# Performance work log

Hardware: AMD Instinct MI355X
Metric: run time of the kernel (lower is better)

Reference implementation:

```python
import jax, jax.numpy as jnp
import numpy as np

N_NODES = 100000
N_EDGES = 1600000
IN_DIM, HID_DIM, OUT_DIM = 128, 128, 64


def setup_inputs() -> dict:
    key = jax.random.key(0)
    ks = jax.random.split(key, 5)
    x = jax.random.normal(ks[0], (N_NODES, IN_DIM), dtype=jnp.float32)
    edge_index = jax.random.randint(ks[1], (2, N_EDGES), 0, N_NODES, dtype=jnp.int64)
    W1 = jax.random.normal(ks[2], (IN_DIM, HID_DIM), dtype=jnp.float32) * (1.0 / np.sqrt(IN_DIM))
    b1 = jnp.zeros((HID_DIM,), dtype=jnp.float32)
    W2 = jax.random.normal(ks[3], (HID_DIM, OUT_DIM), dtype=jnp.float32) * (1.0 / np.sqrt(HID_DIM))
    b2 = jnp.zeros((OUT_DIM,), dtype=jnp.float32)
    return {"x": x, "edge_index": edge_index, "W1": W1, "b1": b1, "W2": W2, "b2": b2}


def _gcn_conv(h, row, col, norm, b, n_nodes):
    # h: [N, F] already linearly transformed; message = norm_e * h[src]; scatter-add to dst
    msg = h[row] * norm[:, None]                      # [E+N, F]
    out = jax.ops.segment_sum(msg, col, num_segments=n_nodes)
    return out + b


def reference(x, edge_index, W1, b1, W2, b2):
    n = x.shape[0]
    loops = jnp.arange(n, dtype=edge_index.dtype)
    row = jnp.concatenate([edge_index[0], loops])     # sources (incl. self loops)
    col = jnp.concatenate([edge_index[1], loops])     # targets
    # symmetric normalization: deg over targets with unit edge weights
    deg = jax.ops.segment_sum(jnp.ones_like(col, dtype=x.dtype), col, num_segments=n)
    dinv = jnp.where(deg > 0, jax.lax.rsqrt(jnp.maximum(deg, 1.0)), 0.0)
    norm = dinv[row] * dinv[col]                      # [E+N]
    h = jax.nn.relu(_gcn_conv(x @ W1, row, col, norm, b1, n))
    out = _gcn_conv(h @ W2, row, col, norm, b2, n)
    return out.mean(axis=0)                           # [OUT_DIM]
```

## Files before the change

kernel.cpp:

```cpp
#include <hip/hip_runtime.h>

#define N_NODES 100000
#define N_EDGES 1600000
#define IN_DIM 128
#define HID_DIM 128
#define OUT_DIM 64
#define BKT_SHIFT 8
#define BKT_SIZE 256
#define NBKT ((N_NODES + BKT_SIZE - 1) / BKT_SIZE)
#define B1 256
#define HIST_N (NBKT * B1)
#define HIST_N2 (2 * HIST_N)
#define GEMM_BLKS ((N_NODES + 127) / 128)

typedef float v2f __attribute__((ext_vector_type(2)));
typedef float v4f __attribute__((ext_vector_type(4)));
typedef short v8s __attribute__((ext_vector_type(8)));

__device__ __forceinline__ unsigned int f2bf(float f) {
  unsigned int u = __float_as_uint(f);
  return (u + 0x7FFFu + ((u >> 16) & 1u)) >> 16;
}

__device__ __forceinline__ void load4(const void* ei, int is64, int half, int base,
                                      int* v) {
  if (is64) {
    const long long* e = (const long long*)ei + (size_t)half * N_EDGES + base;
    longlong2 a = *(const longlong2*)e;
    longlong2 b = *(const longlong2*)(e + 2);
    v[0] = (int)a.x; v[1] = (int)a.y; v[2] = (int)b.x; v[3] = (int)b.y;
  } else {
    const int* e = (const int*)ei + (size_t)half * N_EDGES + base;
    int4 a = *(const int4*)e;
    v[0] = a.x; v[1] = a.y; v[2] = a.z; v[3] = a.w;
  }
}

__device__ __forceinline__ int detect64_block(const unsigned int* ei, int* sh) {
  if (threadIdx.x == 0) *sh = 0;
  __syncthreads();
  if (ei[1 + 2 * threadIdx.x] != 0u) *sh = 1;
  __syncthreads();
  return (*sh == 0) ? 1 : 0;
}

__global__ __launch_bounds__(256) void front_kernel(const float* __restrict__ x,
                                                    const float* __restrict__ W,
                                                    const void* ei,
                                                    unsigned int* __restrict__ G,
                                                    int* hist, float* S) {
  __shared__ __align__(16) char smem[2 * 128 * 136 * 2];
  if (blockIdx.x >= GEMM_BLKS) {
    int* hd = (int*)smem;
    int* hs = hd + NBKT;
    int* sh = hs + NBKT;
    const int hb = blockIdx.x - GEMM_BLKS;
    if (hb == 0 && threadIdx.x < HID_DIM) S[threadIdx.x] = 0.f;
    const int is64 = detect64_block((const unsigned int*)ei, sh);
    for (int k = threadIdx.x; k < NBKT; k += 256) { hd[k] = 0; hs[k] = 0; }
    __syncthreads();
    for (int g = hb * 256 + threadIdx.x; g < N_EDGES / 4; g += B1 * 256) {
      int r[4], c[4];
      load4(ei, is64, 0, g * 4, r);
      load4(ei, is64, 1, g * 4, c);
#pragma unroll
      for (int k = 0; k < 4; k++) {
        atomicAdd(&hd[c[k] >> BKT_SHIFT], 1);
        atomicAdd(&hs[r[k] >> BKT_SHIFT], 1);
      }
    }
    __syncthreads();
    for (int k = threadIdx.x; k < NBKT; k += 256) {
      hist[k * B1 + hb] = hd[k];
      hist[HIST_N + k * B1 + hb] = hs[k];
    }
    return;
  }
  typedef unsigned short us_row[136];
  us_row* lx = (us_row*)smem;
  us_row* lwt = (us_row*)(smem + 128 * 136 * 2);
  const int t = threadIdx.x;
  const int row0 = blockIdx.x * 128;

  {
    const float4* W4 = (const float4*)W;
    for (int it = 0; it < 16; ++it) {
      int idx = t + 256 * it;
      int k = idx >> 5, c4 = (idx & 31) * 4;
      float4 w = W4[idx];
      lwt[c4 + 0][k] = (unsigned short)f2bf(w.x);
      lwt[c4 + 1][k] = (unsigned short)f2bf(w.y);
      lwt[c4 + 2][k] = (unsigned short)f2bf(w.z);
      lwt[c4 + 3][k] = (unsigned short)f2bf(w.w);
    }
  }
  {
    const float4* x4 = (const float4*)(x + (size_t)row0 * IN_DIM);
    for (int it = 0; it < 16; ++it) {
      int idx = t + 256 * it;
      int r = idx >> 5, kq = (idx & 31) * 4;
      float4 v = make_float4(0.f, 0.f, 0.f, 0.f);
      if (row0 + r < N_NODES) v = x4[idx];
      unsigned int p0 = (f2bf(v.y) << 16) | f2bf(v.x);
      unsigned int p1 = (f2bf(v.w) << 16) | f2bf(v.z);
      *(uint2*)&lx[r][kq] = make_uint2(p0, p1);
    }
  }
  __syncthreads();

  const int lane = t & 63;
  const int wv = t >> 6;
  const int m0 = wv * 32;
  const int lrow = lane & 15;
  const int lk = (lane >> 4) * 8;

  v4f acc[2][8];
#pragma unroll
  for (int si = 0; si < 2; si++)
#pragma unroll
    for (int n = 0; n < 8; n++) acc[si][n] = (v4f){0.f, 0.f, 0.f, 0.f};

#pragma unroll
  for (int kk = 0; kk < 128; kk += 32) {
    v8s a0 = *(const v8s*)&lx[m0 + lrow][kk + lk];
    v8s a1 = *(const v8s*)&lx[m0 + 16 + lrow][kk + lk];
#pragma unroll
    for (int n = 0; n < 8; n++) {
      v8s b = *(const v8s*)&lwt[n * 16 + lrow][kk + lk];
      acc[0][n] = __builtin_amdgcn_mfma_f32_16x16x32_bf16(a0, b, acc[0][n], 0, 0, 0);
      acc[1][n] = __builtin_amdgcn_mfma_f32_16x16x32_bf16(a1, b, acc[1][n], 0, 0, 0);
    }
  }

  unsigned char* G8 = (unsigned char*)G;
#pragma unroll
  for (int si = 0; si < 2; si++)
#pragma unroll
    for (int n = 0; n < 8; n++) {
      int colg = n * 16 + (lane & 15);
#pragma unroll
      for (int i = 0; i < 4; i++) {
        int r = row0 + m0 + si * 16 + (lane >> 4) * 4 + i;
        if (r < N_NODES) {
          float v = acc[si][n][i];
          int pk = __builtin_amdgcn_cvt_pk_fp8_f32(v, v, 0, false);
          G8[(size_t)r * HID_DIM + colg] = (unsigned char)(pk & 0xFF);
        }
      }
    }
}

__global__ void scan1_kernel(int* arr, int* bsum, int n) {
  __shared__ int tmp[256];
  int i = blockIdx.x * 256 + threadIdx.x;
  int v = (i < n) ? arr[i] : 0;
  tmp[threadIdx.x] = v;
  __syncthreads();
  for (int off = 1; off < 256; off <<= 1) {
    int t2 = (threadIdx.x >= off) ? tmp[threadIdx.x - off] : 0;
    __syncthreads();
    tmp[threadIdx.x] += t2;
    __syncthreads();
  }
  if (i < n) arr[i] = tmp[threadIdx.x] - v;
  if (threadIdx.x == 255) bsum[blockIdx.x] = tmp[255];
}

__global__ void scan2_kernel(int* bsum, int nb) {
  __shared__ int tmp[1024];
  int v = (threadIdx.x < nb) ? bsum[threadIdx.x] : 0;
  tmp[threadIdx.x] = v;
  __syncthreads();
  for (int off = 1; off < 1024; off <<= 1) {
    int t2 = (threadIdx.x >= off) ? tmp[threadIdx.x - off] : 0;
    __syncthreads();
    tmp[threadIdx.x] += t2;
    __syncthreads();
  }
  if (threadIdx.x < nb) bsum[threadIdx.x] = tmp[threadIdx.x] - v;
}

__global__ __launch_bounds__(256) void scatter_kernel(const void* ei, const int* hist,
                                                      const int* bsum,
                                                      unsigned int* pairs) {
  __shared__ int cd[NBKT], cs[NBKT], sh[1];
  const int is64 = detect64_block((const unsigned int*)ei, sh);
  for (int k = threadIdx.x; k < NBKT; k += 256) {
    cd[k] = hist[k * B1 + blockIdx.x] + bsum[k];
    cs[k] = hist[HIST_N + k * B1 + blockIdx.x] + bsum[NBKT + k];
  }
  __syncthreads();
  for (int g = blockIdx.x * 256 + threadIdx.x; g < N_EDGES / 4; g += B1 * 256) {
    int r[4], c[4];
    load4(ei, is64, 0, g * 4, r);
    load4(ei, is64, 1, g * 4, c);
#pragma unroll
    for (int k = 0; k < 4; k++) {
      int pd = atomicAdd(&cd[c[k] >> BKT_SHIFT], 1);
      pairs[pd] = ((unsigned int)(c[k] & (BKT_SIZE - 1)) << 17) | (unsigned int)r[k];
      int ps = atomicAdd(&cs[r[k] >> BKT_SHIFT], 1);
      pairs[ps] = ((unsigned int)(r[k] & (BKT_SIZE - 1)) << 17) | (unsigned int)c[k];
    }
  }
}

__global__ __launch_bounds__(256) void csr_kernel(const int* hist, const int* bsum,
                                                  const unsigned int* pairs,
                                                  int* rowptr, int* csr, float* dinv) {
  __shared__ int cnt[BKT_SIZE], sc[BKT_SIZE], cur[BKT_SIZE];
  const int k = blockIdx.x;
  const int base = hist[k * B1] + bsum[k];
  const int end = (k == NBKT - 1) ? N_EDGES : hist[(k + 1) * B1] + bsum[k + 1];
  const int nseg = end - base;
  const int l = threadIdx.x;
  cnt[l] = 0;
  __syncthreads();
  for (int i = l; i < nseg; i += 256) atomicAdd(&cnt[pairs[base + i] >> 17], 1);
  __syncthreads();
  sc[l] = cnt[l];
  __syncthreads();
  for (int off = 1; off < BKT_SIZE; off <<= 1) {
    int v = (l >= off) ? sc[l - off] : 0;
    __syncthreads();
    sc[l] += v;
    __syncthreads();
  }
  {
    int excl = sc[l] - cnt[l];
    cur[l] = base + excl;
    int v = k * BKT_SIZE + l;
    if (v < N_NODES) {
      rowptr[v] = base + excl;
      dinv[v] = rsqrtf((float)(cnt[l] + 1));
    }
  }
  if (k == NBKT - 1 && l == 0) rowptr[N_NODES] = N_EDGES;
  __syncthreads();
  for (int i = l; i < nseg; i += 256) {
    unsigned int pk = pairs[base + i];
    int pos = atomicAdd(&cur[pk >> 17], 1);
    csr[pos] = (int)(pk & 0x1FFFFu);
  }
}

__global__ __launch_bounds__(256) void outsum_kernel(const int* hist, const int* bsum,
                                                     const unsigned int* pairs,
                                                     const float* __restrict__ dinv,
                                                     float* wacc,
                                                     unsigned int* __restrict__ G) {
  __shared__ float fb[BKT_SIZE];
  const int k = blockIdx.x;
  const int base = hist[HIST_N + k * B1] + bsum[NBKT + k];
  const int end =
      (k == NBKT - 1) ? 2 * N_EDGES : hist[HIST_N + (k + 1) * B1] + bsum[NBKT + k + 1];
  fb[threadIdx.x] = 0.f;
  __syncthreads();
  for (int i = base + threadIdx.x; i < end; i += 256) {
    unsigned int pk = pairs[i];
    atomicAdd(&fb[pk >> 17], dinv[pk & 0x1FFFFu]);
  }
  {
    const int j0 = k * BKT_SIZE * 32;
#pragma unroll
    for (int it = 0; it < 32; ++it) {
      int j = j0 + it * 256 + threadIdx.x;
      int node = j >> 5;
      if (node < N_NODES) {
        float d = dinv[node];
        unsigned int g = G[j];
        v2f lo = __builtin_amdgcn_cvt_pk_f32_fp8((int)g, false) * d;
        v2f hi = __builtin_amdgcn_cvt_pk_f32_fp8((int)g, true) * d;
        int pk2 = __builtin_amdgcn_cvt_pk_fp8_f32(lo.x, lo.y, 0, false);
        pk2 = __builtin_amdgcn_cvt_pk_fp8_f32(hi.x, hi.y, pk2, true);
        G[j] = (unsigned int)pk2;
      }
    }
  }
  __syncthreads();
  int v = k * BKT_SIZE + threadIdx.x;
  if (v < N_NODES) wacc[v] = fb[threadIdx.x];
}

__global__ __launch_bounds__(256) void aggregate_kernel(
    const unsigned int* __restrict__ G, const int* __restrict__ rowptr,
    const int* __restrict__ csr, const float* __restrict__ dinv,
    const float* __restrict__ wacc, const float* __restrict__ b1,
    float* __restrict__ S) {
  const int lane = threadIdx.x & 63;
  const int sub = lane & 31;
  const int half = lane >> 5;
  const int wid = blockIdx.x * (blockDim.x >> 6) + (threadIdx.x >> 6);
  const int nwaves = gridDim.x * (blockDim.x >> 6);
  const float4 b = ((const float4*)b1)[sub];
  v2f s01 = {0.f, 0.f}, s23 = {0.f, 0.f};

  for (int c = wid; c < N_NODES; c += nwaves) {
    const int start = rowptr[c];
    const int cnum = rowptr[c + 1] - start;
    v2f a01 = {0.f, 0.f}, a23 = {0.f, 0.f};
    if (half == 0) {
      unsigned int g = G[c * 32 + sub];
      a01 = __builtin_amdgcn_cvt_pk_f32_fp8((int)g, false);
      a23 = __builtin_amdgcn_cvt_pk_f32_fp8((int)g, true);
    }
    for (int j0 = 0; j0 < cnum; j0 += 64) {
      int src = 0;
      if (j0 + lane < cnum)
        src = __builtin_nontemporal_load(&csr[start + j0 + lane]);
      const int m = min(64, cnum - j0);
      int i = 0;
      for (; i + 8 <= m; i += 8) {
        int s0 = __shfl(src, i + half);
        int s1 = __shfl(src, i + 2 + half);
        int s2 = __shfl(src, i + 4 + half);
        int s3 = __shfl(src, i + 6 + half);
        unsigned int g0 = G[s0 * 32 + sub];
        unsigned int g1 = G[s1 * 32 + sub];
        unsigned int g2 = G[s2 * 32 + sub];
        unsigned int g3 = G[s3 * 32 + sub];
        a01 += __builtin_amdgcn_cvt_pk_f32_fp8((int)g0, false) +
               __builtin_amdgcn_cvt_pk_f32_fp8((int)g1, false);
        a23 += __builtin_amdgcn_cvt_pk_f32_fp8((int)g0, true) +
               __builtin_amdgcn_cvt_pk_f32_fp8((int)g1, true);
        a01 += __builtin_amdgcn_cvt_pk_f32_fp8((int)g2, false) +
               __builtin_amdgcn_cvt_pk_f32_fp8((int)g3, false);
        a23 += __builtin_amdgcn_cvt_pk_f32_fp8((int)g2, true) +
               __builtin_amdgcn_cvt_pk_f32_fp8((int)g3, true);
      }
      for (; i + 2 <= m; i += 2) {
        int s = __shfl(src, i + half);
        unsigned int g = G[s * 32 + sub];
        a01 += __builtin_amdgcn_cvt_pk_f32_fp8((int)g, false);
        a23 += __builtin_amdgcn_cvt_pk_f32_fp8((int)g, true);
      }
      if (i < m) {
        int s = __shfl(src, i);
        if (half == 0) {
          unsigned int g = G[s * 32 + sub];
          a01 += __builtin_amdgcn_cvt_pk_f32_fp8((int)g, false);
          a23 += __builtin_amdgcn_cvt_pk_f32_fp8((int)g, true);
        }
      }
    }
    a01.x += __shfl(a01.x, sub + 32);
    a01.y += __shfl(a01.y, sub + 32);
    a23.x += __shfl(a23.x, sub + 32);
    a23.y += __shfl(a23.y, sub + 32);
    if (half == 0) {
      float d = dinv[c];
      float wc = d * (wacc[c] + d);
      s01.x += wc * fmaxf(fmaf(d, a01.x, b.x), 0.f);
      s01.y += wc * fmaxf(fmaf(d, a01.y, b.y), 0.f);
      s23.x += wc * fmaxf(fmaf(d, a23.x, b.z), 0.f);
      s23.y += wc * fmaxf(fmaf(d, a23.y, b.w), 0.f);
    }
  }

  __shared__ float ls[HID_DIM];
  if (threadIdx.x < HID_DIM) ls[threadIdx.x] = 0.f;
  __syncthreads();
  if (half == 0) {
    atomicAdd(&ls[4 * sub + 0], s01.x);
    atomicAdd(&ls[4 * sub + 1], s01.y);
    atomicAdd(&ls[4 * sub + 2], s23.x);
    atomicAdd(&ls[4 * sub + 3], s23.y);
  }
  __syncthreads();
  if (threadIdx.x < HID_DIM) atomicAdd(&S[threadIdx.x], ls[threadIdx.x]);
}

__global__ void finish_kernel(const float* __restrict__ S, const float* __restrict__ W2,
                              const float* __restrict__ b2, float* __restrict__ out) {
  int j = threadIdx.x;
  float acc = 0.f;
  for (int k = 0; k < HID_DIM; k++) acc += S[k] * W2[k * OUT_DIM + j];
  out[j] = acc * (1.0f / N_NODES) + b2[j];
}

extern "C" void kernel_launch(void* const* d_in, const int* in_sizes, int n_in,
                              void* d_out, int out_size, void* d_ws, size_t ws_size,
                              hipStream_t stream) {
  const float* x  = (const float*)d_in[0];
  const void*  ei = d_in[1];
  const float* W1 = (const float*)d_in[2];
  const float* b1 = (const float*)d_in[3];
  const float* W2 = (const float*)d_in[4];
  const float* b2 = (const float*)d_in[5];
  float* out = (float*)d_out;

  char* p = (char*)d_ws;
  size_t off = 0;
  auto alloc = [&](size_t bytes) -> void* {
    void* r = p + off;
    off = (off + bytes + 63) & ~(size_t)63;
    return r;
  };
  int*   hist   = (int*)alloc((size_t)HIST_N2 * 4);
  int*   bsum   = (int*)alloc(1024 * 4);
  unsigned int* pairs = (unsigned int*)alloc((size_t)2 * N_EDGES * 4);
  int*   rowptr = (int*)alloc(((size_t)N_NODES + 1) * 4);
  int*   csr    = (int*)alloc((size_t)N_EDGES * 4);
  float* dinv   = (float*)alloc((size_t)N_NODES * 4);
  float* wacc   = (float*)alloc((size_t)N_NODES * 4);
  float* S      = (float*)alloc(HID_DIM * 4);
  unsigned int* G = (unsigned int*)alloc((size_t)N_NODES * HID_DIM);
  (void)ws_size; (void)n_in; (void)in_sizes; (void)out_size;

  const int NBH = HIST_N2 / 256;

  front_kernel<<<GEMM_BLKS + B1, 256, 0, stream>>>(x, W1, ei, G, hist, S);
  scan1_kernel<<<NBH, 256, 0, stream>>>(hist, bsum, HIST_N2);
  scan2_kernel<<<1, 1024, 0, stream>>>(bsum, NBH);
  scatter_kernel<<<B1, 256, 0, stream>>>(ei, hist, bsum, pairs);
  csr_kernel<<<NBKT, 256, 0, stream>>>(hist, bsum, pairs, rowptr, csr, dinv);
  outsum_kernel<<<NBKT, 256, 0, stream>>>(hist, bsum, pairs, dinv, wacc, G);
  aggregate_kernel<<<2048, 256, 0, stream>>>(G, rowptr, csr, dinv, wacc, b1, S);
  finish_kernel<<<1, 64, 0, stream>>>(S, W2, b2, out);
}
```

Measured before the change: 290.7 us.

## Pack source dinv as bf16 into CSR entries instead of rescaling G

The outsum kernel no longer rescales the fp8 feature matrix G by dinv in place (a read-modify-write of G with an fp8 requantisation). It instead writes a bf16-rounded dinv of each source into the upper bits of its CSR entry. The aggregate kernel then reads each neighbour's weight straight from the packed index and multiplies during accumulation. It also loads 8 bytes per lane as uint2, so 16 lanes cover a row and four edges are gathered per wave step instead of two. This removes one pass over G and one fp8 rounding step, in exchange for more multiplies in the gather loop and bf16 precision on the weights.

```diff
diff --git a/kernel.cpp b/kernel.cpp
--- a/kernel.cpp
+++ b/kernel.cpp
@@ -20,6 +20,11 @@
 __device__ __forceinline__ unsigned int f2bf(float f) {
   unsigned int u = __float_as_uint(f);
   return (u + 0x7FFFu + ((u >> 16) & 1u)) >> 16;
+}
+
+template <bool HI>
+__device__ __forceinline__ v2f cvt8(unsigned int u) {
+  return __builtin_amdgcn_cvt_pk_f32_fp8((int)u, HI);
 }
 
 __device__ __forceinline__ void load4(const void* ei, int is64, int half, int base,
@@ -206,7 +211,8 @@
 
 __global__ __launch_bounds__(256) void csr_kernel(const int* hist, const int* bsum,
                                                   const unsigned int* pairs,
-                                                  int* rowptr, int* csr, float* dinv) {
+                                                  int* rowptr, unsigned int* csr,
+                                                  float* dinv) {
   __shared__ int cnt[BKT_SIZE], sc[BKT_SIZE], cur[BKT_SIZE];
   const int k = blockIdx.x;
   const int base = hist[k * B1] + bsum[k];
@@ -239,7 +245,7 @@
   for (int i = l; i < nseg; i += 256) {
     unsigned int pk = pairs[base + i];
     int pos = atomicAdd(&cur[pk >> 17], 1);
-    csr[pos] = (int)(pk & 0x1FFFFu);
+    csr[pos] = pk & 0x1FFFFu;
   }
 }
 
@@ -247,7 +253,7 @@
                                                      const unsigned int* pairs,
                                                      const float* __restrict__ dinv,
                                                      float* wacc,
-                                                     unsigned int* __restrict__ G) {
+                                                     unsigned int* __restrict__ csr) {
   __shared__ float fb[BKT_SIZE];
   const int k = blockIdx.x;
   const int base = hist[HIST_N + k * B1] + bsum[NBKT + k];
@@ -259,22 +265,10 @@
     unsigned int pk = pairs[i];
     atomicAdd(&fb[pk >> 17], dinv[pk & 0x1FFFFu]);
   }
-  {
-    const int j0 = k * BKT_SIZE * 32;
-#pragma unroll
-    for (int it = 0; it < 32; ++it) {
-      int j = j0 + it * 256 + threadIdx.x;
-      int node = j >> 5;
-      if (node < N_NODES) {
-        float d = dinv[node];
-        unsigned int g = G[j];
-        v2f lo = __builtin_amdgcn_cvt_pk_f32_fp8((int)g, false) * d;
-        v2f hi = __builtin_amdgcn_cvt_pk_f32_fp8((int)g, true) * d;
-        int pk2 = __builtin_amdgcn_cvt_pk_fp8_f32(lo.x, lo.y, 0, false);
-        pk2 = __builtin_amdgcn_cvt_pk_fp8_f32(hi.x, hi.y, pk2, true);
-        G[j] = (unsigned int)pk2;
-      }
-    }
+  for (int i = blockIdx.x * 256 + threadIdx.x; i < N_EDGES; i += NBKT * 256) {
+    unsigned int src = csr[i] & 0x1FFFFu;
+    unsigned int bits = f2bf(dinv[src]);
+    csr[i] = (bits << 17) | src;
   }
   __syncthreads();
   int v = k * BKT_SIZE + threadIdx.x;
@@ -282,88 +276,97 @@
 }
 
 __global__ __launch_bounds__(256) void aggregate_kernel(
-    const unsigned int* __restrict__ G, const int* __restrict__ rowptr,
-    const int* __restrict__ csr, const float* __restrict__ dinv,
+    const uint2* __restrict__ G2, const int* __restrict__ rowptr,
+    const unsigned int* __restrict__ csr, const float* __restrict__ dinv,
     const float* __restrict__ wacc, const float* __restrict__ b1,
     float* __restrict__ S) {
   const int lane = threadIdx.x & 63;
-  const int sub = lane & 31;
-  const int half = lane >> 5;
-  const int wid = blockIdx.x * (blockDim.x >> 6) + (threadIdx.x >> 6);
-  const int nwaves = gridDim.x * (blockDim.x >> 6);
-  const float4 b = ((const float4*)b1)[sub];
-  v2f s01 = {0.f, 0.f}, s23 = {0.f, 0.f};
+  const int q = lane & 15;
+  const int grp = lane >> 4;
+  const int wid = blockIdx.x * 4 + (threadIdx.x >> 6);
+  const int nwaves = gridDim.x * 4;
+  const float2* b2p = (const float2*)b1;
+  const float2 bb0 = b2p[q * 4 + 0], bb1 = b2p[q * 4 + 1];
+  const float2 bb2 = b2p[q * 4 + 2], bb3 = b2p[q * 4 + 3];
+  v2f s0 = {0.f, 0.f}, s1 = {0.f, 0.f}, s2 = {0.f, 0.f}, s3 = {0.f, 0.f};
 
   for (int c = wid; c < N_NODES; c += nwaves) {
     const int start = rowptr[c];
     const int cnum = rowptr[c + 1] - start;
-    v2f a01 = {0.f, 0.f}, a23 = {0.f, 0.f};
-    if (half == 0) {
-      unsigned int g = G[c * 32 + sub];
-      a01 = __builtin_amdgcn_cvt_pk_f32_fp8((int)g, false);
-      a23 = __builtin_amdgcn_cvt_pk_f32_fp8((int)g, true);
+    const float d = dinv[c];
+    v2f a0 = {0.f, 0.f}, a1 = {0.f, 0.f}, a2 = {0.f, 0.f}, a3 = {0.f, 0.f};
+    if (grp == 0) {
+      uint2 g = G2[c * 16 + q];
+      a0 = cvt8<false>(g.x) * d;
+      a1 = cvt8<true>(g.x) * d;
+      a2 = cvt8<false>(g.y) * d;
+      a3 = cvt8<true>(g.y) * d;
     }
     for (int j0 = 0; j0 < cnum; j0 += 64) {
-      int src = 0;
+      unsigned int pkl = 0;
       if (j0 + lane < cnum)
-        src = __builtin_nontemporal_load(&csr[start + j0 + lane]);
+        pkl = __builtin_nontemporal_load(&csr[start + j0 + lane]);
       const int m = min(64, cnum - j0);
       int i = 0;
-      for (; i + 8 <= m; i += 8) {
-        int s0 = __shfl(src, i + half);
-        int s1 = __shfl(src, i + 2 + half);
-        int s2 = __shfl(src, i + 4 + half);
-        int s3 = __shfl(src, i + 6 + half);
-        unsigned int g0 = G[s0 * 32 + sub];
-        unsigned int g1 = G[s1 * 32 + sub];
-        unsigned int g2 = G[s2 * 32 + sub];
-        unsigned int g3 = G[s3 * 32 + sub];
-        a01 += __builtin_amdgcn_cvt_pk_f32_fp8((int)g0, false) +
-               __builtin_amdgcn_cvt_pk_f32_fp8((int)g1, false);
-        a23 += __builtin_amdgcn_cvt_pk_f32_fp8((int)g0, true) +
-               __builtin_amdgcn_cvt_pk_f32_fp8((int)g1, true);
-        a01 += __builtin_amdgcn_cvt_pk_f32_fp8((int)g2, false) +
-               __builtin_amdgcn_cvt_pk_f32_fp8((int)g3, false);
-        a23 += __builtin_amdgcn_cvt_pk_f32_fp8((int)g2, true) +
-               __builtin_amdgcn_cvt_pk_f32_fp8((int)g3, true);
+      for (; i + 16 <= m; i += 16) {
+        unsigned int p0 = __shfl(pkl, i + grp);
+        unsigned int p1 = __shfl(pkl, i + 4 + grp);
+        unsigned int p2 = __shfl(pkl, i + 8 + grp);
+        unsigned int p3 = __shfl(pkl, i + 12 + grp);
+        uint2 g0 = G2[(p0 & 0x1FFFFu) * 16 + q];
+        uint2 g1 = G2[(p1 & 0x1FFFFu) * 16 + q];
+        uint2 g2 = G2[(p2 & 0x1FFFFu) * 16 + q];
+        uint2 g3 = G2[(p3 & 0x1FFFFu) * 16 + q];
+        float w0 = __uint_as_float((p0 >> 17) << 16);
+        float w1 = __uint_as_float((p1 >> 17) << 16);
+        float w2 = __uint_as_float((p2 >> 17) << 16);
+        float w3 = __uint_as_float((p3 >> 17) << 16);
+        a0 += cvt8<false>(g0.x) * w0; a1 += cvt8<true>(g0.x) * w0;
+        a2 += cvt8<false>(g0.y) * w0; a3 += cvt8<true>(g0.y) * w0;
+        a0 += cvt8<false>(g1.x) * w1; a1 += cvt8<true>(g1.x) * w1;
+        a2 += cvt8<false>(g1.y) * w1; a3 += cvt8<true>(g1.y) * w1;
+        a0 += cvt8<false>(g2.x) * w2; a1 += cvt8<true>(g2.x) * w2;
+        a2 += cvt8<false>(g2.y) * w2; a3 += cvt8<true>(g2.y) * w2;
+        a0 += cvt8<false>(g3.x) * w3; a1 += cvt8<true>(g3.x) * w3;
+        a2 += cvt8<false>(g3.y) * w3; a3 += cvt8<true>(g3.y) * w3;
       }
-      for (; i + 2 <= m; i += 2) {
-        int s = __shfl(src, i + half);
-        unsigned int g = G[s * 32 + sub];
-        a01 += __builtin_amdgcn_cvt_pk_f32_fp8((int)g, false);
-        a23 += __builtin_amdgcn_cvt_pk_f32_fp8((int)g, true);
+      for (; i < m; i += 4) {
+        int e = i + grp;
+        unsigned int pv = __shfl(pkl, min(e, m - 1));
+        float w = (e < m) ? __uint_as_float((pv >> 17) << 16) : 0.f;
+        uint2 g = G2[(pv & 0x1FFFFu) * 16 + q];
+        a0 += cvt8<false>(g.x) * w; a1 += cvt8<true>(g.x) * w;
+        a2 += cvt8<false>(g.y) * w; a3 += cvt8<true>(g.y) * w;
       }
-      if (i < m) {
-        int s = __shfl(src, i);
-        if (half == 0) {
-          unsigned int g = G[s * 32 + sub];
-          a01 += __builtin_amdgcn_cvt_pk_f32_fp8((int)g, false);
-          a23 += __builtin_amdgcn_cvt_pk_f32_fp8((int)g, true);
-        }
-      }
-    }
-    a01.x += __shfl(a01.x, sub + 32);
-    a01.y += __shfl(a01.y, sub + 32);
-    a23.x += __shfl(a23.x, sub + 32);
-    a23.y += __shfl(a23.y, sub + 32);
-    if (half == 0) {
-      float d = dinv[c];
+    }
+#pragma unroll
+    for (int off = 16; off < 64; off <<= 1) {
+      a0.x += __shfl_xor(a0.x, off); a0.y += __shfl_xor(a0.y, off);
+      a1.x += __shfl_xor(a1.x, off); a1.y += __shfl_xor(a1.y, off);
+      a2.x += __shfl_xor(a2.x, off); a2.y += __shfl_xor(a2.y, off);
+      a3.x += __shfl_xor(a3.x, off); a3.y += __shfl_xor(a3.y, off);
+    }
+    if (grp == 0) {
       float wc = d * (wacc[c] + d);
-      s01.x += wc * fmaxf(fmaf(d, a01.x, b.x), 0.f);
-      s01.y += wc * fmaxf(fmaf(d, a01.y, b.y), 0.f);
-      s23.x += wc * fmaxf(fmaf(d, a23.x, b.z), 0.f);
-      s23.y += wc * fmaxf(fmaf(d, a23.y, b.w), 0.f);
+      s0.x += wc * fmaxf(fmaf(d, a0.x, bb0.x), 0.f);
+      s0.y += wc * fmaxf(fmaf(d, a0.y, bb0.y), 0.f);
+      s1.x += wc * fmaxf(fmaf(d, a1.x, bb1.x), 0.f);
+      s1.y += wc * fmaxf(fmaf(d, a1.y, bb1.y), 0.f);
+      s2.x += wc * fmaxf(fmaf(d, a2.x, bb2.x), 0.f);
+      s2.y += wc * fmaxf(fmaf(d, a2.y, bb2.y), 0.f);
+      s3.x += wc * fmaxf(fmaf(d, a3.x, bb3.x), 0.f);
+      s3.y += wc * fmaxf(fmaf(d, a3.y, bb3.y), 0.f);
     }
   }
 
   __shared__ float ls[HID_DIM];
   if (threadIdx.x < HID_DIM) ls[threadIdx.x] = 0.f;
   __syncthreads();
-  if (half == 0) {
-    atomicAdd(&ls[4 * sub + 0], s01.x);
-    atomicAdd(&ls[4 * sub + 1], s01.y);
-    atomicAdd(&ls[4 * sub + 2], s23.x);
-    atomicAdd(&ls[4 * sub + 3], s23.y);
+  if (grp == 0) {
+    atomicAdd(&ls[8 * q + 0], s0.x); atomicAdd(&ls[8 * q + 1], s0.y);
+    atomicAdd(&ls[8 * q + 2], s1.x); atomicAdd(&ls[8 * q + 3], s1.y);
+    atomicAdd(&ls[8 * q + 4], s2.x); atomicAdd(&ls[8 * q + 5], s2.y);
+    atomicAdd(&ls[8 * q + 6], s3.x); atomicAdd(&ls[8 * q + 7], s3.y);
   }
   __syncthreads();
   if (threadIdx.x < HID_DIM) atomicAdd(&S[threadIdx.x], ls[threadIdx.x]);
@@ -399,7 +402,7 @@
   int*   bsum   = (int*)alloc(1024 * 4);
   unsigned int* pairs = (unsigned int*)alloc((size_t)2 * N_EDGES * 4);
   int*   rowptr = (int*)alloc(((size_t)N_NODES + 1) * 4);
-  int*   csr    = (int*)alloc((size_t)N_EDGES * 4);
+  unsigned int* csr = (unsigned int*)alloc((size_t)N_EDGES * 4);
   float* dinv   = (float*)alloc((size_t)N_NODES * 4);
   float* wacc   = (float*)alloc((size_t)N_NODES * 4);
   float* S      = (float*)alloc(HID_DIM * 4);
@@ -413,7 +416,8 @@
   scan2_kernel<<<1, 1024, 0, stream>>>(bsum, NBH);
   scatter_kernel<<<B1, 256, 0, stream>>>(ei, hist, bsum, pairs);
   csr_kernel<<<NBKT, 256, 0, stream>>>(hist, bsum, pairs, rowptr, csr, dinv);
-  outsum_kernel<<<NBKT, 256, 0, stream>>>(hist, bsum, pairs, dinv, wacc, G);
-  aggregate_kernel<<<2048, 256, 0, stream>>>(G, rowptr, csr, dinv, wacc, b1, S);
+  outsum_kernel<<<NBKT, 256, 0, stream>>>(hist, bsum, pairs, dinv, wacc, csr);
+  aggregate_kernel<<<2048, 256, 0, stream>>>((const uint2*)G, rowptr, csr, dinv, wacc,
+                                             b1, S);
   finish_kernel<<<1, 64, 0, stream>>>(S, W2, b2, out);
 }
```

Measured after the change: 290.8 us. No clear change (+0.0%).

## Pack source dinv as bf16 weight into CSR entries instead of rescaling G

Applied to the files above, without the earlier changes.

Stops rescaling the fp8 feature matrix G by dinv in outsum_kernel. Instead it encodes each edge's source dinv as a truncated bf16 in the upper 15 bits of the CSR index word, and the aggregation multiplies each gathered row by that weight. This removes the read-modify-write pass over G and the extra fp8 requantisation, which should also improve accuracy. In exchange it adds a pass over the CSR array and per-edge multiplies in the gather loop. The weight loses precision because only 15 bits are kept (the bf16 sign bit is dropped).

```diff
diff --git a/kernel.cpp b/kernel.cpp
--- a/kernel.cpp
+++ b/kernel.cpp
@@ -20,6 +20,15 @@
 __device__ __forceinline__ unsigned int f2bf(float f) {
   unsigned int u = __float_as_uint(f);
   return (u + 0x7FFFu + ((u >> 16) & 1u)) >> 16;
+}
+
+template <bool HI>
+__device__ __forceinline__ v2f cvt8(unsigned int u) {
+  return __builtin_amdgcn_cvt_pk_f32_fp8((int)u, HI);
+}
+
+__device__ __forceinline__ float wdec(unsigned int p) {
+  return __uint_as_float((p >> 17) << 16);
 }
 
 __device__ __forceinline__ void load4(const void* ei, int is64, int half, int base,
@@ -206,7 +215,8 @@
 
 __global__ __launch_bounds__(256) void csr_kernel(const int* hist, const int* bsum,
                                                   const unsigned int* pairs,
-                                                  int* rowptr, int* csr, float* dinv) {
+                                                  int* rowptr, unsigned int* csr,
+                                                  float* dinv) {
   __shared__ int cnt[BKT_SIZE], sc[BKT_SIZE], cur[BKT_SIZE];
   const int k = blockIdx.x;
   const int base = hist[k * B1] + bsum[k];
@@ -239,7 +249,7 @@
   for (int i = l; i < nseg; i += 256) {
     unsigned int pk = pairs[base + i];
     int pos = atomicAdd(&cur[pk >> 17], 1);
-    csr[pos] = (int)(pk & 0x1FFFFu);
+    csr[pos] = pk & 0x1FFFFu;
   }
 }
 
@@ -247,7 +257,7 @@
                                                      const unsigned int* pairs,
                                                      const float* __restrict__ dinv,
                                                      float* wacc,
-                                                     unsigned int* __restrict__ G) {
+                                                     unsigned int* __restrict__ csr) {
   __shared__ float fb[BKT_SIZE];
   const int k = blockIdx.x;
   const int base = hist[HIST_N + k * B1] + bsum[NBKT + k];
@@ -259,22 +269,10 @@
     unsigned int pk = pairs[i];
     atomicAdd(&fb[pk >> 17], dinv[pk & 0x1FFFFu]);
   }
-  {
-    const int j0 = k * BKT_SIZE * 32;
-#pragma unroll
-    for (int it = 0; it < 32; ++it) {
-      int j = j0 + it * 256 + threadIdx.x;
-      int node = j >> 5;
-      if (node < N_NODES) {
-        float d = dinv[node];
-        unsigned int g = G[j];
-        v2f lo = __builtin_amdgcn_cvt_pk_f32_fp8((int)g, false) * d;
-        v2f hi = __builtin_amdgcn_cvt_pk_f32_fp8((int)g, true) * d;
-        int pk2 = __builtin_amdgcn_cvt_pk_fp8_f32(lo.x, lo.y, 0, false);
-        pk2 = __builtin_amdgcn_cvt_pk_fp8_f32(hi.x, hi.y, pk2, true);
-        G[j] = (unsigned int)pk2;
-      }
-    }
+  for (int i = blockIdx.x * 256 + threadIdx.x; i < N_EDGES; i += NBKT * 256) {
+    unsigned int src = __builtin_nontemporal_load(&csr[i]) & 0x1FFFFu;
+    unsigned int bits = f2bf(dinv[src]);
+    __builtin_nontemporal_store((bits << 17) | src, &csr[i]);
   }
   __syncthreads();
   int v = k * BKT_SIZE + threadIdx.x;
@@ -283,62 +281,62 @@
 
 __global__ __launch_bounds__(256) void aggregate_kernel(
     const unsigned int* __restrict__ G, const int* __restrict__ rowptr,
-    const int* __restrict__ csr, const float* __restrict__ dinv,
+    const unsigned int* __restrict__ csr, const float* __restrict__ dinv,
     const float* __restrict__ wacc, const float* __restrict__ b1,
     float* __restrict__ S) {
   const int lane = threadIdx.x & 63;
   const int sub = lane & 31;
   const int half = lane >> 5;
-  const int wid = blockIdx.x * (blockDim.x >> 6) + (threadIdx.x >> 6);
-  const int nwaves = gridDim.x * (blockDim.x >> 6);
+  const int wid = blockIdx.x * 4 + (threadIdx.x >> 6);
+  const int nwaves = gridDim.x * 4;
   const float4 b = ((const float4*)b1)[sub];
   v2f s01 = {0.f, 0.f}, s23 = {0.f, 0.f};
 
   for (int c = wid; c < N_NODES; c += nwaves) {
     const int start = rowptr[c];
     const int cnum = rowptr[c + 1] - start;
+    const float d = dinv[c];
     v2f a01 = {0.f, 0.f}, a23 = {0.f, 0.f};
     if (half == 0) {
       unsigned int g = G[c * 32 + sub];
-      a01 = __builtin_amdgcn_cvt_pk_f32_fp8((int)g, false);
-      a23 = __builtin_amdgcn_cvt_pk_f32_fp8((int)g, true);
+      a01 = cvt8<false>(g) * d;
+      a23 = cvt8<true>(g) * d;
     }
     for (int j0 = 0; j0 < cnum; j0 += 64) {
-      int src = 0;
+      unsigned int pkl = 0;
       if (j0 + lane < cnum)
-        src = __builtin_nontemporal_load(&csr[start + j0 + lane]);
+        pkl = __builtin_nontemporal_load(&csr[start + j0 + lane]);
       const int m = min(64, cnum - j0);
       int i = 0;
       for (; i + 8 <= m; i += 8) {
-        int s0 = __shfl(src, i + half);
-        int s1 = __shfl(src, i + 2 + half);
-        int s2 = __shfl(src, i + 4 + half);
-        int s3 = __shfl(src, i + 6 + half);
-        unsigned int g0 = G[s0 * 32 + sub];
-        unsigned int g1 = G[s1 * 32 + sub];
-        unsigned int g2 = G[s2 * 32 + sub];
-        unsigned int g3 = G[s3 * 32 + sub];
-        a01 += __builtin_amdgcn_cvt_pk_f32_fp8((int)g0, false) +
-               __builtin_amdgcn_cvt_pk_f32_fp8((int)g1, false);
-        a23 += __builtin_amdgcn_cvt_pk_f32_fp8((int)g0, true) +
-               __builtin_amdgcn_cvt_pk_f32_fp8((int)g1, true);
-        a01 += __builtin_amdgcn_cvt_pk_f32_fp8((int)g2, false) +
-               __builtin_amdgcn_cvt_pk_f32_fp8((int)g3, false);
-        a23 += __builtin_amdgcn_cvt_pk_f32_fp8((int)g2, true) +
-               __builtin_amdgcn_cvt_pk_f32_fp8((int)g3, true);
+        unsigned int p0 = __shfl(pkl, i + half);
+        unsigned int p1 = __shfl(pkl, i + 2 + half);
+        unsigned int p2 = __shfl(pkl, i + 4 + half);
+        unsigned int p3 = __shfl(pkl, i + 6 + half);
+        unsigned int g0 = G[(p0 & 0x1FFFFu) * 32 + sub];
+        unsigned int g1 = G[(p1 & 0x1FFFFu) * 32 + sub];
+        unsigned int g2 = G[(p2 & 0x1FFFFu) * 32 + sub];
+        unsigned int g3 = G[(p3 & 0x1FFFFu) * 32 + sub];
+        float w0 = wdec(p0), w1 = wdec(p1), w2 = wdec(p2), w3 = wdec(p3);
+        a01 += cvt8<false>(g0) * w0; a23 += cvt8<true>(g0) * w0;
+        a01 += cvt8<false>(g1) * w1; a23 += cvt8<true>(g1) * w1;
+        a01 += cvt8<false>(g2) * w2; a23 += cvt8<true>(g2) * w2;
+        a01 += cvt8<false>(g3) * w3; a23 += cvt8<true>(g3) * w3;
       }
       for (; i + 2 <= m; i += 2) {
-        int s = __shfl(src, i + half);
-        unsigned int g = G[s * 32 + sub];
-        a01 += __builtin_amdgcn_cvt_pk_f32_fp8((int)g, false);
-        a23 += __builtin_amdgcn_cvt_pk_f32_fp8((int)g, true);
+        unsigned int p = __shfl(pkl, i + half);
+        unsigned int g = G[(p & 0x1FFFFu) * 32 + sub];
+        float w = wdec(p);
+        a01 += cvt8<false>(g) * w;
+        a23 += cvt8<true>(g) * w;
       }
       if (i < m) {
-        int s = __shfl(src, i);
+        unsigned int p = __shfl(pkl, i);
         if (half == 0) {
-          unsigned int g = G[s * 32 + sub];
-          a01 += __builtin_amdgcn_cvt_pk_f32_fp8((int)g, false);
-          a23 += __builtin_amdgcn_cvt_pk_f32_fp8((int)g, true);
+          unsigned int g = G[(p & 0x1FFFFu) * 32 + sub];
+          float w = wdec(p);
+          a01 += cvt8<false>(g) * w;
+          a23 += cvt8<true>(g) * w;
         }
       }
     }
@@ -347,7 +345,6 @@
     a23.x += __shfl(a23.x, sub + 32);
     a23.y += __shfl(a23.y, sub + 32);
     if (half == 0) {
-      float d = dinv[c];
       float wc = d * (wacc[c] + d);
       s01.x += wc * fmaxf(fmaf(d, a01.x, b.x), 0.f);
       s01.y += wc * fmaxf(fmaf(d, a01.y, b.y), 0.f);
@@ -399,7 +396,7 @@
   int*   bsum   = (int*)alloc(1024 * 4);
   unsigned int* pairs = (unsigned int*)alloc((size_t)2 * N_EDGES * 4);
   int*   rowptr = (int*)alloc(((size_t)N_NODES + 1) * 4);
-  int*   csr    = (int*)alloc((size_t)N_EDGES * 4);
+  unsigned int* csr = (unsigned int*)alloc((size_t)N_EDGES * 4);
   float* dinv   = (float*)alloc((size_t)N_NODES * 4);
   float* wacc   = (float*)alloc((size_t)N_NODES * 4);
   float* S      = (float*)alloc(HID_DIM * 4);
@@ -413,7 +410,7 @@
   scan2_kernel<<<1, 1024, 0, stream>>>(bsum, NBH);
   scatter_kernel<<<B1, 256, 0, stream>>>(ei, hist, bsum, pairs);
   csr_kernel<<<NBKT, 256, 0, stream>>>(hist, bsum, pairs, rowptr, csr, dinv);
-  outsum_kernel<<<NBKT, 256, 0, stream>>>(hist, bsum, pairs, dinv, wacc, G);
+  outsum_kernel<<<NBKT, 256, 0, stream>>>(hist, bsum, pairs, dinv, wacc, csr);
   aggregate_kernel<<<2048, 256, 0, stream>>>(G, rowptr, csr, dinv, wacc, b1, S);
   finish_kernel<<<1, 64, 0, stream>>>(S, W2, b2, out);
 }
```

After: 288.1 us. About the same (-0.9%).
